# Optimization experiments

Hardware: AMD Instinct MI355X
Metric: run time of the kernel (lower is better)

The kernel has to match this reference:

```python
import jax, jax.numpy as jnp
import numpy as np
import math

B, T, N, C = 16, 24, 207, 64
E = 16   # embedding_dim
L = 3    # num_layers
NH = 4   # temporal attention heads
HD = C // NH
HOR = 12 # horizon


def _ln(x, w, b, eps=1e-5):
    m = x.mean(-1, keepdims=True)
    v = ((x - m) ** 2).mean(-1, keepdims=True)
    return (x - m) / jnp.sqrt(v + eps) * w + b


def setup_inputs():
    ks = iter(jax.random.split(jax.random.key(0), 64))
    def g(shape, s=0.1):
        return jax.random.normal(next(ks), shape, dtype=jnp.float32) * s
    inp = {}
    inp['x'] = jax.random.normal(next(ks), (B, T, N, 4), dtype=jnp.float32)
    adj = (jax.random.uniform(next(ks), (N, N)) < 0.3).astype(jnp.float32)
    inp['static_adj'] = jnp.maximum(adj, jnp.eye(N, dtype=jnp.float32))  # self-loops: no all-zero rows
    inp['node_embedding'] = g((N, E), 1.0)
    for nm in ['hour', 'day', 'weekend']:
        inp[nm + '_w'] = g((E, 1)); inp[nm + '_b'] = g((E,))
    inp['in_w'] = g((C, 1 + 4 * E)); inp['in_b'] = g((C,))
    C8 = C // 8
    inp['sa_qw'] = g((L, C8, C)); inp['sa_qb'] = g((L, C8))
    inp['sa_kw'] = g((L, C8, C)); inp['sa_kb'] = g((L, C8))
    inp['sa_vw'] = g((L, C, C)); inp['sa_vb'] = g((L, C))
    for nm in ['ta_q', 'ta_k', 'ta_v', 'ta_o']:
        inp[nm + 'w'] = g((L, C, C)); inp[nm + 'b'] = g((L, C))
    inp['ln1_w'] = jnp.ones((L, C)); inp['ln1_b'] = jnp.zeros((L, C))
    inp['ln2_w'] = jnp.ones((L, C)); inp['ln2_b'] = jnp.zeros((L, C))
    inp['ffn_w1'] = g((L, 4 * C, C)); inp['ffn_b1'] = g((L, 4 * C))
    inp['ffn_w2'] = g((L, C, 4 * C)); inp['ffn_b2'] = g((L, C))
    inp['gru_wih'] = g((2, 3 * C, C)); inp['gru_whh'] = g((2, 3 * C, C))
    inp['gru_bih'] = g((2, 3 * C)); inp['gru_bhh'] = g((2, 3 * C))
    inp['pred_w'] = g((HOR, C * T), 0.02); inp['pred_b'] = g((HOR,))
    return inp


def _forward(x, static_adj, node_embedding, hour_w, hour_b, day_w, day_b, weekend_w, weekend_b, in_w, in_b, sa_qw, sa_qb, sa_kw, sa_kb, sa_vw, sa_vb, ta_qw, ta_qb, ta_kw, ta_kb, ta_vw, ta_vb, ta_ow, ta_ob, ln1_w, ln1_b, ln2_w, ln2_b, ffn_w1, ffn_b1, ffn_w2, ffn_b2, gru_wih, gru_whh, gru_bih, gru_bhh, pred_w, pred_b):
    # eval mode: dropout = identity, no input perturbation
    flow = x[..., :1]
    hour = x[..., 1:2]; weekend = x[..., 2:3]; day = x[..., 3:4]
    node_emb = jnp.broadcast_to(node_embedding[None, None], (B, T, N, E))
    hour_emb = hour @ hour_w.T + hour_b
    day_emb = day @ day_w.T + day_b
    weekend_emb = weekend @ weekend_w.T + weekend_b
    h = jnp.concatenate([flow, node_emb, hour_emb, day_emb, weekend_emb], axis=-1)  # [B,T,N,65]
    h = h.transpose(0, 3, 2, 1)  # [B,F,N,T]
    h = jnp.einsum('of,bfnt->bont', in_w, h) + in_b[None, :, None, None]  # 1x1 conv -> [B,C,N,T]
    # positional encoding (added along channel/time, matching permute in torch)
    pos = jnp.arange(100, dtype=jnp.float32)[:, None]
    div = jnp.exp(jnp.arange(0, C, 2, dtype=jnp.float32) * (-math.log(10000.0) / C))
    pe = jnp.stack([jnp.sin(pos * div), jnp.cos(pos * div)], axis=-1).reshape(100, C)
    h = h + pe[:T].T[None, :, None, :]
    # F.normalize(adj, p=1, dim=-1) with eps clamp (torch default 1e-12)
    adj_norm = static_adj / jnp.maximum(jnp.abs(static_adj).sum(-1, keepdims=True), 1e-12)
    zero_mask = (adj_norm == 0)[None]  # [1,N,N]
    attn_mats = []
    sqrtC = math.sqrt(C); sqrtHD = math.sqrt(HD)
    for l in range(L):
        # ---- spatial attention (faithful dim-mixing reshapes of the original) ----
        hp = h.transpose(0, 1, 3, 2)  # [B,C,T,N]
        q = jnp.einsum('oc,bctn->botn', sa_qw[l], hp) + sa_qb[l][None, :, None, None]
        k = jnp.einsum('oc,bctn->botn', sa_kw[l], hp) + sa_kb[l][None, :, None, None]
        v = jnp.einsum('oc,bctn->botn', sa_vw[l], hp) + sa_vb[l][None, :, None, None]
        C8 = q.shape[1]
        q2 = q.reshape(B * T, C8, N).transpose(0, 2, 1)
        k2 = k.reshape(B * T, C8, N)
        v2 = v.reshape(B * T, C, N)
        attn = jax.nn.softmax(jnp.einsum('bnc,bcm->bnm', q2, k2) / sqrtC, axis=-1)
        attn = jnp.where(zero_mask, -jnp.inf, attn)
        attn = jax.nn.softmax(attn, axis=-1)
        sp = jnp.einsum('bcn,bmn->bcm', v2, attn).reshape(B, T, C, N).transpose(0, 2, 3, 1)  # [B,C,N,T]
        attn_mats.append(attn.reshape(B, T, N, N))
        h = h + sp
        h = _ln(h.transpose(0, 3, 2, 1), ln1_w[l], ln1_b[l]).transpose(0, 3, 2, 1)
        # ---- temporal attention (multi-head over time, per node) ----
        xt = h.transpose(0, 2, 3, 1)  # [B,N,T,C]
        def heads(w, b):
            return (xt @ w.T + b).reshape(B, N, T, NH, HD).transpose(0, 1, 3, 2, 4)
        tq = heads(ta_qw[l], ta_qb[l]); tk = heads(ta_kw[l], ta_kb[l]); tv = heads(ta_vw[l], ta_vb[l])
        scores = jnp.einsum('bnhtd,bnhsd->bnhts', tq, tk) / sqrtHD
        ta = jnp.einsum('bnhts,bnhsd->bnhtd', jax.nn.softmax(scores, axis=-1), tv)
        ta = ta.transpose(0, 1, 3, 2, 4).reshape(B, N, T, C) @ ta_ow[l].T + ta_ob[l]
        h = h + ta.transpose(0, 3, 1, 2)
        # ---- LN2 + FFN (residual taken post-LN2, as in the original) ----
        hl = _ln(h.transpose(0, 3, 2, 1), ln2_w[l], ln2_b[l])  # [B,T,N,C]
        ffn = jax.nn.relu(hl @ ffn_w1[l].T + ffn_b1[l]) @ ffn_w2[l].T + ffn_b2[l]
        h = (hl + ffn).transpose(0, 3, 2, 1)
    # ---- 2-layer GRU over time per (batch, node) ----
    seq = h.transpose(0, 2, 3, 1).reshape(B * N, T, C).transpose(1, 0, 2)  # [T,BN,C]
    for l in range(2):
        xp = jnp.einsum('tbc,gc->tbg', seq, gru_wih[l]) + gru_bih[l]
        whh = gru_whh[l]; bhh = gru_bhh[l]
        def step(hprev, xg):
            hg = hprev @ whh.T + bhh
            r = jax.nn.sigmoid(xg[:, :C] + hg[:, :C])
            z = jax.nn.sigmoid(xg[:, C:2 * C] + hg[:, C:2 * C])
            n = jnp.tanh(xg[:, 2 * C:] + r * hg[:, 2 * C:])
            hnew = (1 - z) * n + z * hprev
            return hnew, hnew
        _, seq = jax.lax.scan(step, jnp.zeros((B * N, C), dtype=seq.dtype), xp)
    h = seq.transpose(1, 0, 2).reshape(B, N, T, C).transpose(0, 3, 1, 2)  # [B,C,N,T]
    # ---- prediction head ----
    flat = h.transpose(0, 2, 1, 3).reshape(B * N, C * T)
    out = (flat @ pred_w.T + pred_b).reshape(B, N, HOR).transpose(0, 2, 1)  # [B,HOR,N]
    return out, attn_mats


def reference(x, static_adj, node_embedding, hour_w, hour_b, day_w, day_b, weekend_w, weekend_b, in_w, in_b, sa_qw, sa_qb, sa_kw, sa_kb, sa_vw, sa_vb, ta_qw, ta_qb, ta_kw, ta_kb, ta_vw, ta_vb, ta_ow, ta_ob, ln1_w, ln1_b, ln2_w, ln2_b, ffn_w1, ffn_b1, ffn_w2, ffn_b2, gru_wih, gru_whh, gru_bih, gru_bhh, pred_w, pred_b):
    out, attn_mats = _forward(x, static_adj, node_embedding, hour_w, hour_b, day_w, day_b, weekend_w, weekend_b, in_w, in_b, sa_qw, sa_qb, sa_kw, sa_kb, sa_vw, sa_vb, ta_qw, ta_qb, ta_kw, ta_kb, ta_vw, ta_vb, ta_ow, ta_ob, ln1_w, ln1_b, ln2_w, ln2_b, ffn_w1, ffn_b1, ffn_w2, ffn_b2, gru_wih, gru_whh, gru_bih, gru_bhh, pred_w, pred_b)
    return (out, jnp.stack(attn_mats))
```

## Files before the change

### kernel.cpp

```cpp
#include <hip/hip_runtime.h>
#include <math.h>

namespace {

constexpr int B = 16, T = 24, N = 207, C = 64, HOR = 12;
constexpr int BT = B * T;
constexpr int BN = B * N;
constexpr int P = B * T * N;
constexpr int NC = N * C;

constexpr size_t H_OFF = 0;
constexpr size_t A_OFF = 5087232;
constexpr size_t Q_OFF = A_OFF + 5087232;
constexpr size_t K_OFF = Q_OFF + 635904;
constexpr size_t B_OFF = K_OFF + 635904;
constexpr size_t WS_FLOATS = B_OFF + 20348928;

constexpr size_t EP_OFF = 17000000;
constexpr size_t PK_OFF = 18000000;

__device__ __forceinline__ float wsum(float v) {
#pragma unroll
  for (int off = 32; off; off >>= 1) v += __shfl_xor(v, off);
  return v;
}
__device__ __forceinline__ float wmax(float v) {
#pragma unroll
  for (int off = 32; off; off >>= 1) v = fmaxf(v, __shfl_xor(v, off));
  return v;
}

__global__ __launch_bounds__(256) void k_embed_pack(
    const float* __restrict__ nodee, const float* __restrict__ hw,
    const float* __restrict__ hb, const float* __restrict__ dw,
    const float* __restrict__ db, const float* __restrict__ ww,
    const float* __restrict__ wb, const float* __restrict__ inw,
    const float* __restrict__ inb, float* __restrict__ ep) {
  int e = blockIdx.x * 256 + threadIdx.x;
  if (e < 13248) {
    int n = e >> 6, c = e & 63;
    const float* w = inw + c * 65 + 1;
    float a = 0.f;
#pragma unroll
    for (int i = 0; i < 16; i++) a += w[i] * nodee[n * 16 + i];
    ep[e] = a;
  } else if (e < 13568) {
    int m = e - 13248;
    int which = m >> 6, c = m & 63;
    const float* w = inw + c * 65;
    float r = 0.f;
    if (which == 0) {
      r = w[0];
    } else if (which == 1) {
#pragma unroll
      for (int i = 0; i < 16; i++) r += w[17 + i] * hw[i];
    } else if (which == 2) {
#pragma unroll
      for (int i = 0; i < 16; i++) r += w[33 + i] * dw[i];
    } else if (which == 3) {
#pragma unroll
      for (int i = 0; i < 16; i++) r += w[49 + i] * ww[i];
    } else {
      r = inb[c];
#pragma unroll
      for (int i = 0; i < 16; i++)
        r += w[17 + i] * hb[i] + w[33 + i] * db[i] + w[49 + i] * wb[i];
    }
    ep[e] = r;
  } else if (e < 15104) {
    int m = e - 13568;
    int t = m >> 6, c = m & 63;
    float dv = expf((float)(c & ~1) * (-9.210340371976184f / 64.0f));
    float ang = (float)t * dv;
    ep[e] = (c & 1) ? cosf(ang) : sinf(ang);
  }
}

__global__ __launch_bounds__(256) void k_embed(
    const float* __restrict__ x, const float* __restrict__ ep,
    float* __restrict__ H) {
  int pos = blockIdx.x * 4 + (threadIdx.x >> 6);
  int c = threadIdx.x & 63;
  int n = pos % N;
  int t = (pos / N) % T;
  const float* xv = x + (size_t)pos * 4;
  float flow = xv[0], hour = xv[1], wkend = xv[2], day = xv[3];
  float acc = ep[13504 + c] + ep[13248 + c] * flow + ep[13312 + c] * hour +
              ep[13376 + c] * day + ep[13440 + c] * wkend + ep[n * 64 + c] +
              ep[13568 + t * 64 + c];
  H[(size_t)pos * 64 + c] = acc;
}

__global__ __launch_bounds__(256) void k_pack_all(
    const float* __restrict__ w1, const float* __restrict__ w2,
    const float* __restrict__ tqw, const float* __restrict__ tkw,
    const float* __restrict__ tvw, const float* __restrict__ tow,
    float* __restrict__ pk) {
  int e = blockIdx.x * 256 + threadIdx.x;
  int l = e / 49152;
  int m = e % 49152;
  float* w1t = pk + l * 49152;
  float* w2q = w1t + 16384;
  float* taq = w2q + 16384;
  if (m < 16384) {
    int c = m >> 8, j = m & 255;
    w1t[m] = w1[l * 16384 + j * 64 + c];
  } else if (m < 32768) {
    int mm = m - 16384;
    int jq = mm >> 8, c = (mm & 255) >> 2, kk = mm & 3;
    w2q[mm] = w2[l * 16384 + c * 256 + jq * 4 + kk];
  } else {
    int m2 = m - 32768;
    int ph = m2 >> 12;
    int mm = m2 & 4095;
    int cq = mm >> 8, o = (mm & 255) >> 2, j = mm & 3;
    const float* src =
        (ph == 0 ? tqw : ph == 1 ? tkw : ph == 2 ? tvw : tow) + l * 4096;
    taq[ph * 4096 + mm] = src[o * 64 + 4 * cq + j];
  }
}

__global__ __launch_bounds__(256) void k_spatial_qkv(
    const float* __restrict__ H, const float* __restrict__ qw,
    const float* __restrict__ qb, const float* __restrict__ kw,
    const float* __restrict__ kb, const float* __restrict__ vw,
    const float* __restrict__ vb, float* __restrict__ q, float* __restrict__ k,
    float* __restrict__ v, int l) {
  __shared__ float hs[N * 65];
  int g = blockIdx.x;
  int b = g / T, t = g % T;
  const float* Hbt = H + (size_t)g * NC;
  for (int e = threadIdx.x; e < NC; e += 256) {
    int n = e >> 6, c = e & 63;
    hs[n * 65 + c] = Hbt[e];
  }
  __syncthreads();
  qw += l * 8 * 64; qb += l * 8;
  kw += l * 8 * 64; kb += l * 8;
  vw += l * 64 * 64; vb += l * 64;
  for (int e = threadIdx.x; e < 16 * N; e += 256) {
    int o = e / N, n = e % N;
    int oo = o & 7;
    const float* W = (o < 8 ? qw : kw) + oo * 64;
    float acc = (o < 8 ? qb : kb)[oo];
#pragma unroll
    for (int c = 0; c < 64; c++) acc += W[c] * hs[n * 65 + c];
    size_t oidx = ((size_t)(b * 8 + oo) * T + t) * N + n;
    if (o < 8) q[oidx] = acc; else k[oidx] = acc;
  }
  for (int e = threadIdx.x; e < 64 * N; e += 256) {
    int o = e / N, n = e % N;
    const float* W = vw + o * 64;
    float acc = vb[o];
#pragma unroll
    for (int c = 0; c < 64; c++) acc += W[c] * hs[n * 65 + c];
    v[((size_t)(b * 64 + o) * T + t) * N + n] = acc;
  }
}

__global__ __launch_bounds__(256) void k_spatial_attn(
    const float* __restrict__ q, const float* __restrict__ k,
    const float* __restrict__ adj, float* __restrict__ attn_out) {
  __shared__ float qs[8 * 208], ks[8 * 208];
  int g = blockIdx.x;
  const float* qg = q + (size_t)g * 1656;
  const float* kg = k + (size_t)g * 1656;
  for (int e = threadIdx.x; e < 1656; e += 256) {
    int c2 = e / N, n = e % N;
    qs[c2 * 208 + n] = qg[e];
    ks[c2 * 208 + n] = kg[e];
  }
  __syncthreads();
  int wave = threadIdx.x >> 6, lane = threadIdx.x & 63;
  for (int n = wave; n < N; n += 4) {
    float s[4];
    float mx = -INFINITY;
#pragma unroll
    for (int j = 0; j < 4; j++) {
      int m = lane + 64 * j;
      float acc = -INFINITY;
      if (m < N) {
        acc = 0.f;
#pragma unroll
        for (int c2 = 0; c2 < 8; c2++) acc += qs[c2 * 208 + n] * ks[c2 * 208 + m];
        acc *= 0.125f;
      }
      s[j] = acc;
      mx = fmaxf(mx, acc);
    }
    mx = wmax(mx);
    float sum = 0.f;
#pragma unroll
    for (int j = 0; j < 4; j++) {
      int m = lane + 64 * j;
      float e = (m < N) ? expf(s[j] - mx) : 0.f;
      s[j] = e;
      sum += e;
    }
    sum = wsum(sum);
    float inv = 1.f / sum;
    float mx2 = -INFINITY;
    bool ok[4];
#pragma unroll
    for (int j = 0; j < 4; j++) {
      int m = lane + 64 * j;
      float p = s[j] * inv;
      bool valid = (m < N) && (adj[n * N + m] != 0.0f);
      ok[j] = valid;
      s[j] = p;
      if (valid) mx2 = fmaxf(mx2, p);
    }
    mx2 = wmax(mx2);
    float sum2 = 0.f;
#pragma unroll
    for (int j = 0; j < 4; j++) {
      float e = ok[j] ? expf(s[j] - mx2) : 0.f;
      s[j] = e;
      sum2 += e;
    }
    sum2 = wsum(sum2);
    float inv2 = 1.f / sum2;
    float* orow = attn_out + ((size_t)g * N + n) * N;
#pragma unroll
    for (int j = 0; j < 4; j++) {
      int m = lane + 64 * j;
      if (m < N) orow[m] = s[j] * inv2;
    }
  }
}

__global__ __launch_bounds__(256, 3) void k_spatial_apply(
    const float* __restrict__ v, const float* __restrict__ attn,
    float* __restrict__ H) {
  __shared__ float vs[64 * 207];
  int g = blockIdx.x;
  int ms = blockIdx.y;
  const float* vg = v + (size_t)g * NC;
  for (int e = threadIdx.x; e < NC; e += 256) vs[e] = vg[e];
  __syncthreads();
  int wave = threadIdx.x >> 6, lane = threadIdx.x & 63;
  const float* ag = attn + (size_t)g * (N * N);
  float* Hg = H + (size_t)g * NC;
  int mbeg = ms * 52;
  int mend = min(mbeg + 52, N);
  int m_w = mbeg + wave;
  size_t Dg = (size_t)g * (N * N);
  int p = (int)((4 - ((Dg + (size_t)m_w * N) & 3)) & 3);
  const float* ar[13];
  int mrow[13];
#pragma unroll
  for (int r = 0; r < 13; r++) {
    int m = m_w + 4 * r;
    mrow[r] = m;
    int msafe = (m < N) ? m : m - 4;
    ar[r] = ag + (size_t)msafe * N;
  }
  float acc[13];
#pragma unroll
  for (int r = 0; r < 13; r++) acc[r] = 0.f;
  const float* vrow = vs + lane * 207;
  for (int n = 0; n < p; n++) {
    float vv = vrow[n];
#pragma unroll
    for (int r = 0; r < 13; r++) acc[r] += vv * ar[r][n];
  }
  for (int n4 = 0; n4 < 51; n4++) {
    int n = p + n4 * 4;
    float v0 = vrow[n], v1 = vrow[n + 1], v2 = vrow[n + 2], v3 = vrow[n + 3];
#pragma unroll
    for (int r = 0; r < 13; r++) {
      float4 a = *(const float4*)(ar[r] + n);
      acc[r] += v0 * a.x;
      acc[r] += v1 * a.y;
      acc[r] += v2 * a.z;
      acc[r] += v3 * a.w;
    }
  }
  for (int n = p + 204; n < 207; n++) {
    float vv = vrow[n];
#pragma unroll
    for (int r = 0; r < 13; r++) acc[r] += vv * ar[r][n];
  }
#pragma unroll
  for (int r = 0; r < 13; r++) {
    int m = mrow[r];
    if (m < mend) Hg[(size_t)m * 64 + lane] += acc[r];
  }
}

__global__ __launch_bounds__(256) void k_temporal(
    float* __restrict__ H, const float* __restrict__ taq,
    const float* __restrict__ qb, const float* __restrict__ kb,
    const float* __restrict__ vb, const float* __restrict__ ob,
    const float* __restrict__ lnw, const float* __restrict__ lnb, int l) {
  __shared__ float xs[24 * 68], qs[24 * 68], ks[24 * 68], vs[24 * 68];
  __shared__ float ss[96 * 25];
  int bn = blockIdx.x;
  int b = bn / N, n = bn % N;
  size_t base = ((size_t)b * T * N + n) * 64;
  int lane = threadIdx.x & 63, tg = threadIdx.x >> 6;
  float lw = lnw[l * 64 + lane], lb = lnb[l * 64 + lane];
  for (int t = tg; t < 24; t += 4) {
    float xv = H[base + (size_t)t * NC + lane];
    float mean = wsum(xv) * (1.f / 64.f);
    float d = xv - mean;
    float var = wsum(d * d) * (1.f / 64.f);
    xs[t * 68 + lane] = d / sqrtf(var + 1e-5f) * lw + lb;
  }
  __syncthreads();
  const float4* wq_all = (const float4*)taq;
  const float* Bm[3] = {qb + l * 64, kb + l * 64, vb + l * 64};
  float* Dm[3] = {qs, ks, vs};
#pragma unroll
  for (int ph = 0; ph < 3; ph++) {
    const float4* wq = wq_all + ph * 1024;
    float acc[6];
    float bv = Bm[ph][lane];
#pragma unroll
    for (int i = 0; i < 6; i++) acc[i] = bv;
#pragma unroll 4
    for (int cq = 0; cq < 16; cq++) {
      float4 w = wq[cq * 64 + lane];
#pragma unroll
      for (int i = 0; i < 6; i++) {
        float4 xv = *(const float4*)(&xs[(tg * 6 + i) * 68 + cq * 4]);
        acc[i] += xv.x * w.x + xv.y * w.y + xv.z * w.z + xv.w * w.w;
      }
    }
    float* dst = Dm[ph];
#pragma unroll
    for (int i = 0; i < 6; i++) dst[(tg * 6 + i) * 68 + lane] = acc[i];
  }
  __syncthreads();
  for (int e = threadIdx.x; e < 2304; e += 256) {
    int u = e % 24, t = (e / 24) % 24, h = e / 576;
    float a = 0.f;
#pragma unroll
    for (int dq = 0; dq < 4; dq++) {
      float4 qv = *(const float4*)(&qs[t * 68 + h * 16 + dq * 4]);
      float4 kv = *(const float4*)(&ks[u * 68 + h * 16 + dq * 4]);
      a += qv.x * kv.x + qv.y * kv.y + qv.z * kv.z + qv.w * kv.w;
    }
    ss[(h * 24 + t) * 25 + u] = a * 0.25f;
  }
  __syncthreads();
  if (threadIdx.x < 96) {
    float* row = ss + threadIdx.x * 25;
    float mx = -INFINITY;
#pragma unroll
    for (int u = 0; u < 24; u++) mx = fmaxf(mx, row[u]);
    float sum = 0.f;
#pragma unroll
    for (int u = 0; u < 24; u++) {
      float e2 = expf(row[u] - mx);
      row[u] = e2;
      sum += e2;
    }
    float inv = 1.f / sum;
#pragma unroll
    for (int u = 0; u < 24; u++) row[u] *= inv;
  }
  __syncthreads();
  {
    int h = lane >> 4;
    float acc2[6];
#pragma unroll
    for (int i = 0; i < 6; i++) acc2[i] = 0.f;
    for (int u = 0; u < 24; u++) {
      float vsv = vs[u * 68 + lane];
#pragma unroll
      for (int i = 0; i < 6; i++)
        acc2[i] += ss[(h * 24 + (tg * 6 + i)) * 25 + u] * vsv;
    }
#pragma unroll
    for (int i = 0; i < 6; i++) qs[(tg * 6 + i) * 68 + lane] = acc2[i];
  }
  __syncthreads();
  {
    const float4* wo = wq_all + 3 * 1024;
    float acc[6];
    float bv = ob[l * 64 + lane];
#pragma unroll
    for (int i = 0; i < 6; i++) acc[i] = bv;
#pragma unroll 4
    for (int cq = 0; cq < 16; cq++) {
      float4 w = wo[cq * 64 + lane];
#pragma unroll
      for (int i = 0; i < 6; i++) {
        float4 xv = *(const float4*)(&qs[(tg * 6 + i) * 68 + cq * 4]);
        acc[i] += xv.x * w.x + xv.y * w.y + xv.z * w.z + xv.w * w.w;
      }
    }
#pragma unroll
    for (int i = 0; i < 6; i++)
      H[base + (size_t)(tg * 6 + i) * NC + lane] =
          xs[(tg * 6 + i) * 68 + lane] + acc[i];
  }
}

__global__ __launch_bounds__(256) void k_ffn(
    float* __restrict__ H, const float* __restrict__ lnw,
    const float* __restrict__ lnb, const float* __restrict__ w1t,
    const float* __restrict__ b1, const float* __restrict__ w2q,
    const float* __restrict__ b2, int l) {
  __shared__ float xs[24 * 66];
  __shared__ float hids[24 * 260];
  int bn = blockIdx.x;
  int b = bn / N, n = bn % N;
  size_t base = ((size_t)b * T * N + n) * 64;
  int lane = threadIdx.x & 63, tg = threadIdx.x >> 6;
  for (int t = tg; t < 24; t += 4) {
    float xv = H[base + (size_t)t * NC + lane];
    float mean = wsum(xv) * (1.f / 64.f);
    float d = xv - mean;
    float var = wsum(d * d) * (1.f / 64.f);
    xs[t * 66 + lane] = d / sqrtf(var + 1e-5f) * lnw[l * 64 + lane] + lnb[l * 64 + lane];
  }
  __syncthreads();
  int j0 = lane * 4;
  float4 b4 = *(const float4*)(b1 + l * 256 + j0);
  float a0[6], a1[6], a2[6], a3[6];
#pragma unroll
  for (int i = 0; i < 6; i++) { a0[i] = b4.x; a1[i] = b4.y; a2[i] = b4.z; a3[i] = b4.w; }
  for (int c = 0; c < 64; c++) {
    float4 w4 = *(const float4*)(w1t + c * 256 + j0);
#pragma unroll
    for (int i = 0; i < 6; i++) {
      float xv = xs[(tg * 6 + i) * 66 + c];
      a0[i] += xv * w4.x;
      a1[i] += xv * w4.y;
      a2[i] += xv * w4.z;
      a3[i] += xv * w4.w;
    }
  }
#pragma unroll
  for (int i = 0; i < 6; i++) {
    int t = tg * 6 + i;
    float4 r = make_float4(fmaxf(a0[i], 0.f), fmaxf(a1[i], 0.f),
                           fmaxf(a2[i], 0.f), fmaxf(a3[i], 0.f));
    *(float4*)(&hids[t * 260 + j0]) = r;
  }
  __syncthreads();
  const float4* w2q4 = (const float4*)w2q;
  float acc[6];
#pragma unroll
  for (int i = 0; i < 6; i++) acc[i] = 0.f;
  for (int jq = 0; jq < 64; jq++) {
    float4 w = w2q4[jq * 64 + lane];
#pragma unroll
    for (int i = 0; i < 6; i++) {
      float4 hv = *(const float4*)(&hids[(tg * 6 + i) * 260 + jq * 4]);
      acc[i] += hv.x * w.x + hv.y * w.y + hv.z * w.z + hv.w * w.w;
    }
  }
  float bias = b2[l * 64 + lane];
#pragma unroll
  for (int i = 0; i < 6; i++) {
    int t = tg * 6 + i;
    H[base + (size_t)t * NC + lane] = xs[t * 66 + lane] + bias + acc[i];
  }
}

__global__ __launch_bounds__(256) void k_gru_xp(
    const float* __restrict__ X, const float* __restrict__ wih,
    const float* __restrict__ bih, float* __restrict__ xp, int l) {
  __shared__ float ws_[192 * 65];
  __shared__ float xv[16 * 64];
  int p0 = blockIdx.x * 16;
  for (int e = threadIdx.x; e < 192 * 64; e += 256) {
    int gI = e >> 6, c = e & 63;
    ws_[gI * 65 + c] = wih[l * 12288 + e];
  }
  for (int e = threadIdx.x; e < 16 * 64; e += 256) {
    int s = e >> 6, c = e & 63;
    int p = p0 + s;
    int t = p / BN, bn = p % BN;
    float val;
    if (l == 0) {
      int b = bn / N, n = bn % N;
      val = X[(((size_t)b * T + t) * N + n) * 64 + c];
    } else {
      val = X[(size_t)p * 64 + c];
    }
    xv[e] = val;
  }
  __syncthreads();
  for (int e = threadIdx.x; e < 16 * 192; e += 256) {
    int s = e / 192, gI = e % 192;
    float acc = bih[l * 192 + gI];
#pragma unroll
    for (int c = 0; c < 64; c++) acc += xv[s * 64 + c] * ws_[gI * 65 + c];
    xp[((size_t)(p0 + s)) * 192 + gI] = acc;
  }
}

__global__ __launch_bounds__(256) void k_gru_scan(
    const float* __restrict__ xp, const float* __restrict__ whh,
    const float* __restrict__ bhh, float* __restrict__ seq_out, int l) {
  constexpr int S = 8;
  __shared__ float hprev[S][64];
  __shared__ float hg[3][S][64];
  __shared__ float xpbuf[2][S * 192];
  int bn0 = blockIdx.x * S;
  int lane = threadIdx.x & 63;
  int wv = threadIdx.x >> 6;

  float4 w4[16];
  if (wv < 3) {
    const float* wr = whh + l * 12288 + (wv * 64 + lane) * 64;
#pragma unroll
    for (int j = 0; j < 16; j++) w4[j] = *(const float4*)(wr + j * 4);
  }
  float b_r = bhh[l * 192 + lane];
  float b_z = bhh[l * 192 + 64 + lane];
  float b_n = bhh[l * 192 + 128 + lane];

  for (int e = threadIdx.x; e < S * 64; e += 256) ((float*)hprev)[e] = 0.f;
  {
    const float* src = xp + (size_t)bn0 * 192;
    for (int e = threadIdx.x; e < S * 192; e += 256) xpbuf[0][e] = src[e];
  }
  __syncthreads();

  for (int t = 0; t < T; t++) {
    int cur = t & 1;
    if (wv < 3) {
      float acc[S];
#pragma unroll
      for (int s = 0; s < S; s++) acc[s] = 0.f;
#pragma unroll
      for (int j = 0; j < 16; j++) {
        float4 w = w4[j];
#pragma unroll
        for (int s = 0; s < S; s++) {
          float4 hb = *(const float4*)(&hprev[s][j * 4]);
          acc[s] += w.x * hb.x + w.y * hb.y + w.z * hb.z + w.w * hb.w;
        }
      }
#pragma unroll
      for (int s = 0; s < S; s++) hg[wv][s][lane] = acc[s];
    } else {
      if (t + 1 < T) {
        const float* src = xp + ((size_t)(t + 1) * BN + bn0) * 192;
        float* dst = xpbuf[(t + 1) & 1];
        for (int e = lane * 4; e < S * 192; e += 256) {
          *(float4*)(dst + e) = *(const float4*)(src + e);
        }
      }
    }
    __syncthreads();
#pragma unroll
    for (int ii = 0; ii < 2; ii++) {
      int s = wv + 4 * ii;
      const float* xr = &xpbuf[cur][s * 192];
      float r = 1.f / (1.f + expf(-(xr[lane] + hg[0][s][lane] + b_r)));
      float z = 1.f / (1.f + expf(-(xr[64 + lane] + hg[1][s][lane] + b_z)));
      float nn = tanhf(xr[128 + lane] + r * (hg[2][s][lane] + b_n));
      float hp = hprev[s][lane];
      float hnew = (1.f - z) * nn + z * hp;
      hprev[s][lane] = hnew;
      seq_out[((size_t)t * BN + bn0 + s) * 64 + lane] = hnew;
    }
    __syncthreads();
  }
}

__global__ __launch_bounds__(256) void k_pred(
    const float* __restrict__ seq2, const float* __restrict__ pw,
    const float* __restrict__ pb, float* __restrict__ out) {
  __shared__ float s_[1536];
  int bn = blockIdx.x;
  int b = bn / N, n = bn % N;
  for (int e = threadIdx.x; e < 1536; e += 256) {
    int t = e >> 6, c = e & 63;
    s_[c * 24 + t] = seq2[((size_t)t * BN + bn) * 64 + c];
  }
  __syncthreads();
  int wave = threadIdx.x >> 6, lane = threadIdx.x & 63;
  for (int hor = wave; hor < 12; hor += 4) {
    const float* w = pw + hor * 1536;
    float acc = 0.f;
#pragma unroll 4
    for (int kk = lane; kk < 1536; kk += 64) acc += s_[kk] * w[kk];
    acc = wsum(acc);
    if (lane == 0) out[(size_t)b * (HOR * N) + hor * N + n] = acc + pb[hor];
  }
}

}

extern "C" void kernel_launch(void* const* d_in, const int* in_sizes, int n_in,
                              void* d_out, int out_size, void* d_ws, size_t ws_size,
                              hipStream_t stream) {
  const float* x       = (const float*)d_in[0];
  const float* adj     = (const float*)d_in[1];
  const float* nodee   = (const float*)d_in[2];
  const float* hour_w  = (const float*)d_in[3];
  const float* hour_b  = (const float*)d_in[4];
  const float* day_w   = (const float*)d_in[5];
  const float* day_b   = (const float*)d_in[6];
  const float* wk_w    = (const float*)d_in[7];
  const float* wk_b    = (const float*)d_in[8];
  const float* in_w    = (const float*)d_in[9];
  const float* in_b    = (const float*)d_in[10];
  const float* sa_qw   = (const float*)d_in[11];
  const float* sa_qb   = (const float*)d_in[12];
  const float* sa_kw   = (const float*)d_in[13];
  const float* sa_kb   = (const float*)d_in[14];
  const float* sa_vw   = (const float*)d_in[15];
  const float* sa_vb   = (const float*)d_in[16];
  const float* ta_qw   = (const float*)d_in[17];
  const float* ta_qb   = (const float*)d_in[18];
  const float* ta_kw   = (const float*)d_in[19];
  const float* ta_kb   = (const float*)d_in[20];
  const float* ta_vw   = (const float*)d_in[21];
  const float* ta_vb   = (const float*)d_in[22];
  const float* ta_ow   = (const float*)d_in[23];
  const float* ta_ob   = (const float*)d_in[24];
  const float* ln1_w   = (const float*)d_in[25];
  const float* ln1_b   = (const float*)d_in[26];
  const float* ln2_w   = (const float*)d_in[27];
  const float* ln2_b   = (const float*)d_in[28];
  const float* ffn_w1  = (const float*)d_in[29];
  const float* ffn_b1  = (const float*)d_in[30];
  const float* ffn_w2  = (const float*)d_in[31];
  const float* ffn_b2  = (const float*)d_in[32];
  const float* gru_wih = (const float*)d_in[33];
  const float* gru_whh = (const float*)d_in[34];
  const float* gru_bih = (const float*)d_in[35];
  const float* gru_bhh = (const float*)d_in[36];
  const float* pred_w  = (const float*)d_in[37];
  const float* pred_b  = (const float*)d_in[38];

  if (ws_size < WS_FLOATS * sizeof(float)) return;

  float* ws   = (float*)d_ws;
  float* H    = ws + H_OFF;
  float* bufA = ws + A_OFF;
  float* q    = ws + Q_OFF;
  float* k    = ws + K_OFF;
  float* bufB = ws + B_OFF;

  float* out       = (float*)d_out;
  float* attn_base = out + (size_t)B * HOR * N;

  float* v   = bufB;
  float* xp  = bufB;
  float* ep  = bufB + EP_OFF;
  float* pk  = bufB + PK_OFF;

  k_embed_pack<<<60, 256, 0, stream>>>(nodee, hour_w, hour_b, day_w, day_b,
                                       wk_w, wk_b, in_w, in_b, ep);
  k_embed<<<P / 4, 256, 0, stream>>>(x, ep, H);
  k_pack_all<<<576, 256, 0, stream>>>(ffn_w1, ffn_w2, ta_qw, ta_kw, ta_vw,
                                      ta_ow, pk);

  for (int l = 0; l < 3; l++) {
    float* attn_l = attn_base + (size_t)l * BT * N * N;
    float* w1t = pk + (size_t)l * 49152;
    float* w2q = w1t + 16384;
    float* taq = w2q + 16384;
    k_spatial_qkv<<<BT, 256, 0, stream>>>(H, sa_qw, sa_qb, sa_kw, sa_kb, sa_vw,
                                          sa_vb, q, k, v, l);
    k_spatial_attn<<<BT, 256, 0, stream>>>(q, k, adj, attn_l);
    k_spatial_apply<<<dim3(BT, 4), 256, 0, stream>>>(v, attn_l, H);
    k_temporal<<<BN, 256, 0, stream>>>(H, taq, ta_qb, ta_kb, ta_vb, ta_ob,
                                       ln1_w, ln1_b, l);
    k_ffn<<<BN, 256, 0, stream>>>(H, ln2_w, ln2_b, w1t, ffn_b1, w2q, ffn_b2, l);
  }

  k_gru_xp<<<P / 16, 256, 0, stream>>>(H, gru_wih, gru_bih, xp, 0);
  k_gru_scan<<<BN / 8, 256, 0, stream>>>(xp, gru_whh, gru_bhh, bufA, 0);
  k_gru_xp<<<P / 16, 256, 0, stream>>>(bufA, gru_wih, gru_bih, xp, 1);
  k_gru_scan<<<BN / 8, 256, 0, stream>>>(xp, gru_whh, gru_bhh, H, 1);

  k_pred<<<BN, 256, 0, stream>>>(H, pred_w, pred_b, out);
}
```

Before: 2.142 ms.

## Fuse spatial attention softmax with attention-times-V apply in one kernel

Merges the spatial attention softmax kernel and the separate attention-times-V apply kernel. Each block now loads its V slice into padded LDS. Right after computing a softmax row in registers, it accumulates P·V by broadcasting probabilities across the wave with readlane. This removes the global re-read of the full attention matrix and one launch per layer. In exchange, the grid drops from BT×4 blocks to BT blocks, and the larger LDS footprint limits occupancy. The per-row scalar-broadcast loop may also be latency-bound.

```diff
diff --git a/kernel.cpp b/kernel.cpp
--- a/kernel.cpp
+++ b/kernel.cpp
@@ -28,6 +28,9 @@
 #pragma unroll
   for (int off = 32; off; off >>= 1) v = fmaxf(v, __shfl_xor(v, off));
   return v;
+}
+__device__ __forceinline__ float rdlane(float v, int l) {
+  return __uint_as_float(__builtin_amdgcn_readlane(__float_as_uint(v), l));
 }
 
 __global__ __launch_bounds__(256) void k_embed_pack(
@@ -158,10 +161,12 @@
   }
 }
 
-__global__ __launch_bounds__(256) void k_spatial_attn(
+__global__ __launch_bounds__(256, 2) void k_spatial_attn_pv(
     const float* __restrict__ q, const float* __restrict__ k,
-    const float* __restrict__ adj, float* __restrict__ attn_out) {
+    const float* __restrict__ adj, const float* __restrict__ v,
+    float* __restrict__ attn_out, float* __restrict__ H) {
   __shared__ float qs[8 * 208], ks[8 * 208];
+  __shared__ float vs[64 * 212];
   int g = blockIdx.x;
   const float* qg = q + (size_t)g * 1656;
   const float* kg = k + (size_t)g * 1656;
@@ -170,9 +175,19 @@
     qs[c2 * 208 + n] = qg[e];
     ks[c2 * 208 + n] = kg[e];
   }
+  const float* vg = v + (size_t)g * NC;
+  for (int e = threadIdx.x; e < NC; e += 256) {
+    int c = e / N, n = e % N;
+    vs[c * 212 + n] = vg[e];
+  }
+  for (int e = threadIdx.x; e < 320; e += 256) {
+    int c = e / 5;
+    vs[c * 212 + 207 + (e % 5)] = 0.f;
+  }
   __syncthreads();
   int wave = threadIdx.x >> 6, lane = threadIdx.x & 63;
-  for (int n = wave; n < N; n += 4) {
+  float* Hg = H + (size_t)g * NC;
+  for (int row = wave; row < N; row += 4) {
     float s[4];
     float mx = -INFINITY;
 #pragma unroll
@@ -182,7 +197,8 @@
       if (m < N) {
         acc = 0.f;
 #pragma unroll
-        for (int c2 = 0; c2 < 8; c2++) acc += qs[c2 * 208 + n] * ks[c2 * 208 + m];
+        for (int c2 = 0; c2 < 8; c2++)
+          acc += qs[c2 * 208 + row] * ks[c2 * 208 + m];
         acc *= 0.125f;
       }
       s[j] = acc;
@@ -205,7 +221,7 @@
     for (int j = 0; j < 4; j++) {
       int m = lane + 64 * j;
       float p = s[j] * inv;
-      bool valid = (m < N) && (adj[n * N + m] != 0.0f);
+      bool valid = (m < N) && (adj[row * N + m] != 0.0f);
       ok[j] = valid;
       s[j] = p;
       if (valid) mx2 = fmaxf(mx2, p);
@@ -220,71 +236,40 @@
     }
     sum2 = wsum(sum2);
     float inv2 = 1.f / sum2;
-    float* orow = attn_out + ((size_t)g * N + n) * N;
+    float* orow = attn_out + ((size_t)g * N + row) * N;
 #pragma unroll
     for (int j = 0; j < 4; j++) {
       int m = lane + 64 * j;
       if (m < N) orow[m] = s[j] * inv2;
     }
-  }
-}
-
-__global__ __launch_bounds__(256, 3) void k_spatial_apply(
-    const float* __restrict__ v, const float* __restrict__ attn,
-    float* __restrict__ H) {
-  __shared__ float vs[64 * 207];
-  int g = blockIdx.x;
-  int ms = blockIdx.y;
-  const float* vg = v + (size_t)g * NC;
-  for (int e = threadIdx.x; e < NC; e += 256) vs[e] = vg[e];
-  __syncthreads();
-  int wave = threadIdx.x >> 6, lane = threadIdx.x & 63;
-  const float* ag = attn + (size_t)g * (N * N);
-  float* Hg = H + (size_t)g * NC;
-  int mbeg = ms * 52;
-  int mend = min(mbeg + 52, N);
-  int m_w = mbeg + wave;
-  size_t Dg = (size_t)g * (N * N);
-  int p = (int)((4 - ((Dg + (size_t)m_w * N) & 3)) & 3);
-  const float* ar[13];
-  int mrow[13];
-#pragma unroll
-  for (int r = 0; r < 13; r++) {
-    int m = m_w + 4 * r;
-    mrow[r] = m;
-    int msafe = (m < N) ? m : m - 4;
-    ar[r] = ag + (size_t)msafe * N;
-  }
-  float acc[13];
-#pragma unroll
-  for (int r = 0; r < 13; r++) acc[r] = 0.f;
-  const float* vrow = vs + lane * 207;
-  for (int n = 0; n < p; n++) {
-    float vv = vrow[n];
-#pragma unroll
-    for (int r = 0; r < 13; r++) acc[r] += vv * ar[r][n];
-  }
-  for (int n4 = 0; n4 < 51; n4++) {
-    int n = p + n4 * 4;
-    float v0 = vrow[n], v1 = vrow[n + 1], v2 = vrow[n + 2], v3 = vrow[n + 3];
-#pragma unroll
-    for (int r = 0; r < 13; r++) {
-      float4 a = *(const float4*)(ar[r] + n);
-      acc[r] += v0 * a.x;
-      acc[r] += v1 * a.y;
-      acc[r] += v2 * a.z;
-      acc[r] += v3 * a.w;
-    }
-  }
-  for (int n = p + 204; n < 207; n++) {
-    float vv = vrow[n];
-#pragma unroll
-    for (int r = 0; r < 13; r++) acc[r] += vv * ar[r][n];
-  }
-#pragma unroll
-  for (int r = 0; r < 13; r++) {
-    int m = mrow[r];
-    if (m < mend) Hg[(size_t)m * 64 + lane] += acc[r];
+    const float* vrow = vs + lane * 212;
+    float pacc0 = 0.f, pacc1 = 0.f, pacc2 = 0.f, pacc3 = 0.f;
+#pragma unroll
+    for (int j = 0; j < 3; j++) {
+      float sj = s[j];
+#pragma unroll
+      for (int qq = 0; qq < 16; qq++) {
+        int n4 = j * 16 + qq;
+        float4 vv = *(const float4*)(vrow + n4 * 4);
+        pacc0 += rdlane(sj, 4 * qq) * vv.x;
+        pacc1 += rdlane(sj, 4 * qq + 1) * vv.y;
+        pacc2 += rdlane(sj, 4 * qq + 2) * vv.z;
+        pacc3 += rdlane(sj, 4 * qq + 3) * vv.w;
+      }
+    }
+    {
+      float sj = s[3];
+#pragma unroll
+      for (int qq = 0; qq < 4; qq++) {
+        int n4 = 48 + qq;
+        float4 vv = *(const float4*)(vrow + n4 * 4);
+        pacc0 += rdlane(sj, 4 * qq) * vv.x;
+        pacc1 += rdlane(sj, 4 * qq + 1) * vv.y;
+        pacc2 += rdlane(sj, 4 * qq + 2) * vv.z;
+        pacc3 += rdlane(sj, 4 * qq + 3) * vv.w;
+      }
+    }
+    Hg[(size_t)row * 64 + lane] += inv2 * ((pacc0 + pacc1) + (pacc2 + pacc3));
   }
 }
 
@@ -662,8 +647,7 @@
     float* taq = w2q + 16384;
     k_spatial_qkv<<<BT, 256, 0, stream>>>(H, sa_qw, sa_qb, sa_kw, sa_kb, sa_vw,
                                           sa_vb, q, k, v, l);
-    k_spatial_attn<<<BT, 256, 0, stream>>>(q, k, adj, attn_l);
-    k_spatial_apply<<<dim3(BT, 4), 256, 0, stream>>>(v, attn_l, H);
+    k_spatial_attn_pv<<<BT, 256, 0, stream>>>(q, k, adj, v, attn_l, H);
     k_temporal<<<BN, 256, 0, stream>>>(H, taq, ta_qb, ta_kb, ta_vb, ta_ob,
                                        ln1_w, ln1_b, l);
     k_ffn<<<BN, 256, 0, stream>>>(H, ln2_w, ln2_b, w1t, ffn_b1, w2q, ffn_b2, l);
```

Result: no change. 2.165 ms (+1.1%).
